# Performance work log

Measured on AMD Instinct MI355X. Metric: run time of the kernel, lower is better.

The kernel has to match this reference:

```python
import jax, jax.numpy as jnp
import numpy as np

NEG_INF = -9e15  # matches the torch -9000000000000000.0 mask value
LRELU_SLOPE = 0.01  # torch nn.LeakyReLU default


def setup_inputs() -> dict:
    key = jax.random.key(0)
    k1, k2, k3, k4 = jax.random.split(key, 4)
    N, F_in, F_out = 8192, 256, 128
    x = jax.random.normal(k1, (N, F_in), dtype=jnp.float32)
    adj = jax.random.randint(k2, (N, N), 0, 2, dtype=jnp.int32)
    # xavier_uniform with gain=1.414
    limW = 1.414 * np.sqrt(6.0 / (F_in + F_out))
    W = jax.random.uniform(k3, (F_in, F_out), minval=-limW, maxval=limW, dtype=jnp.float32)
    lima = 1.414 * np.sqrt(6.0 / (2 * F_out + 1))
    a = jax.random.uniform(k4, (2 * F_out, 1), minval=-lima, maxval=lima, dtype=jnp.float32)
    return {"x": x, "adj": adj, "W": W, "a": a}


def reference(x, adj, W, a):
    # h: [N, F_out]
    h = x @ W
    F_out = h.shape[1]
    a1 = a[:F_out, 0]   # attention vector for source node i
    a2 = a[F_out:, 0]   # attention vector for target node j
    # e[i, j] = leaky_relu(h_i . a1 + h_j . a2) -- equivalent to the repeat/cat
    # construction without materializing the [N, N, 2F] tensor.
    e = (h @ a1)[:, None] + (h @ a2)[None, :]  # [N, N]
    e = jnp.where(e > 0, e, LRELU_SLOPE * e)
    scores = jnp.where(adj > 0, e, NEG_INF)
    attention = jax.nn.softmax(scores, axis=1)  # dropout omitted (eval mode)
    h_prime = attention @ h  # [N, F_out]
    return jax.nn.elu(h_prime)
```

## Files before the change

### kernel.cpp

```cpp
#include <hip/hip_runtime.h>
#include <hip/hip_bf16.h>
#include <stdint.h>


#define N_NODES 8192
#define F_INF   256
#define F_OUT   128
#define LRELU   0.01f

typedef __bf16 bf16x8 __attribute__((ext_vector_type(8)));
typedef float  f32x4  __attribute__((ext_vector_type(4)));
using bf16 = __hip_bfloat16;

__device__ __forceinline__ float b2f(bf16 v) { return __bfloat162float(v); }
__device__ __forceinline__ bf16  f2b(float v) { return __float2bfloat16(v); }

__device__ __forceinline__ void gll16(const void* g, void* l) {
    __builtin_amdgcn_global_load_lds(
        (const __attribute__((address_space(1))) uint32_t*)g,
        (__attribute__((address_space(3))) uint32_t*)l, 16, 0, 0);
}

__global__ __launch_bounds__(256) void k_xw(const float* __restrict__ x,
                                            const float* __restrict__ W,
                                            const float* __restrict__ a,
                                            const int* __restrict__ adjp,
                                            bf16* __restrict__ hT,
                                            float* __restrict__ s1,
                                            float* __restrict__ s2,
                                            float* __restrict__ mgp,
                                            uint32_t* __restrict__ mask) {
    __shared__ __align__(16) bf16 WTh[F_OUT][F_INF + 8];
    __shared__ __align__(16) bf16 WTl[F_OUT][F_INF + 8];
    __shared__ __align__(16) bf16 XSh[32][72];
    __shared__ __align__(16) bf16 XSl[32][72];
    __shared__ float a1s[F_OUT], a2s[F_OUT], s1L[32], s2L[32];
    const int tid  = threadIdx.x;
    const int lane = tid & 63, wave = tid >> 6;
    const int i0   = blockIdx.x * 32;
    if (tid < F_OUT) { a1s[tid] = a[tid]; a2s[tid] = a[tid + F_OUT]; }
    if (tid < 32)    { s1L[tid] = 0.f; s2L[tid] = 0.f; }
    for (int idx = tid; idx < (F_INF * F_OUT) / 8; idx += 256) {
        int k  = idx >> 4;
        int n0 = (idx & 15) * 8;
        const float* src = W + (size_t)k * F_OUT + n0;
        float4 va = *(const float4*)(src);
        float4 vb = *(const float4*)(src + 4);
        float v[8] = {va.x, va.y, va.z, va.w, vb.x, vb.y, vb.z, vb.w};
#pragma unroll
        for (int c = 0; c < 8; ++c) {
            bf16 hi = f2b(v[c]);
            WTh[n0 + c][k] = hi;
            WTl[n0 + c][k] = f2b(v[c] - b2f(hi));
        }
    }
    __syncthreads();
    f32x4 acc[4];
#pragma unroll
    for (int t = 0; t < 4; ++t) acc[t] = {0.f, 0.f, 0.f, 0.f};
    const int m = lane & 15, quad = lane >> 4;
    const int rt = wave & 1, cH = wave >> 1;
    for (int kc = 0; kc < F_INF / 64; ++kc) {
        const int k0 = kc * 64;
        {
            int part = tid & 7;
            int r    = tid >> 3;
            const float* src = x + (size_t)(i0 + r) * F_INF + k0 + part * 8;
            float4 va = *(const float4*)(src);
            float4 vb = *(const float4*)(src + 4);
            float v[8] = {va.x, va.y, va.z, va.w, vb.x, vb.y, vb.z, vb.w};
            __align__(16) bf16 th[8];
            __align__(16) bf16 tl[8];
#pragma unroll
            for (int c = 0; c < 8; ++c) {
                bf16 hi = f2b(v[c]);
                th[c] = hi;
                tl[c] = f2b(v[c] - b2f(hi));
            }
            *(uint4*)(&XSh[r][part * 8]) = *(const uint4*)th;
            *(uint4*)(&XSl[r][part * 8]) = *(const uint4*)tl;
        }
        __syncthreads();
#pragma unroll
        for (int ks = 0; ks < 2; ++ks) {
            bf16x8 ah = *(const bf16x8*)(&XSh[rt * 16 + m][ks * 32 + quad * 8]);
            bf16x8 al = *(const bf16x8*)(&XSl[rt * 16 + m][ks * 32 + quad * 8]);
#pragma unroll
            for (int c = 0; c < 4; ++c) {
                const int ct = cH * 4 + c;
                bf16x8 bh = *(const bf16x8*)(&WTh[ct * 16 + m][k0 + ks * 32 + quad * 8]);
                bf16x8 bl = *(const bf16x8*)(&WTl[ct * 16 + m][k0 + ks * 32 + quad * 8]);
                acc[c] = __builtin_amdgcn_mfma_f32_16x16x32_bf16(al, bh, acc[c], 0, 0, 0);
                acc[c] = __builtin_amdgcn_mfma_f32_16x16x32_bf16(ah, bl, acc[c], 0, 0, 0);
                acc[c] = __builtin_amdgcn_mfma_f32_16x16x32_bf16(ah, bh, acc[c], 0, 0, 0);
            }
        }
        __syncthreads();
    }
    float p1[4] = {0.f, 0.f, 0.f, 0.f}, p2[4] = {0.f, 0.f, 0.f, 0.f};
#pragma unroll
    for (int c = 0; c < 4; ++c) {
        const int f = (cH * 4 + c) * 16 + m;
        const float w1 = a1s[f], w2 = a2s[f];
#pragma unroll
        for (int r = 0; r < 4; ++r) { p1[r] += acc[c][r] * w1; p2[r] += acc[c][r] * w2; }
    }
#pragma unroll
    for (int r = 0; r < 4; ++r) {
        const int row = rt * 16 + quad * 4 + r;
        atomicAdd(&s1L[row], p1[r]);
        atomicAdd(&s2L[row], p2[r]);
    }
#pragma unroll
    for (int c = 0; c < 4; ++c) {
        const int f = (cH * 4 + c) * 16 + m;
#pragma unroll
        for (int r = 0; r < 4; ++r) {
            const int i = i0 + rt * 16 + quad * 4 + r;
            hT[(size_t)f * N_NODES + i] = f2b(acc[c][r]);
        }
    }
    __syncthreads();
    if (tid < 32) {
        s1[i0 + tid] = s1L[tid];
        s2[i0 + tid] = s2L[tid];
        float m2 = s2L[tid];
#pragma unroll
        for (int s = 16; s > 0; s >>= 1) m2 = fmaxf(m2, __shfl_xor(m2, s));
        if (tid == 0) mgp[blockIdx.x] = m2;
    }
    {
        const size_t base = (size_t)blockIdx.x * 8192 + tid;
#pragma unroll 2
        for (int k2 = 0; k2 < 32; ++k2) {
            const size_t w = base + (size_t)k2 * 256;
            const int4* p = (const int4*)(adjp + w * 32);
            uint32_t b = 0;
#pragma unroll
            for (int g = 0; g < 8; ++g) {
                int4 v = p[g];
                b |= (uint32_t)(v.x > 0) << (g * 4 + 0);
                b |= (uint32_t)(v.y > 0) << (g * 4 + 1);
                b |= (uint32_t)(v.z > 0) << (g * 4 + 2);
                b |= (uint32_t)(v.w > 0) << (g * 4 + 3);
            }
            mask[w] = b;
        }
    }
}

__global__ __launch_bounds__(256, 4) void k_attn(const uint32_t* __restrict__ mask,
                                                 const float* __restrict__ s1g,
                                                 const float* __restrict__ s2g,
                                                 const float* __restrict__ mgp,
                                                 const bf16* __restrict__ hT,
                                                 float* __restrict__ Of,
                                                 float* __restrict__ lp) {
    __shared__ __align__(16) bf16 HS2[2][F_OUT][64];
    __shared__ float wred[4];
    __shared__ float lsum[32];
    const int tid  = threadIdx.x;
    const int lane = tid & 63, wave = tid >> 6;
    const int m = lane & 15, quad = lane >> 4;
    const int rt = wave & 1, kh = wave >> 1;
    const int i0    = blockIdx.x * 32;
    const int jq    = blockIdx.y;
    const int jbase = jq * 2048;
    const int irow  = i0 + rt * 16 + m;
    const float s1v = s1g[irow];
    float mv = mgp[tid];
#pragma unroll
    for (int s = 32; s > 0; s >>= 1) mv = fmaxf(mv, __shfl_xor(mv, s));
    if (lane == 0) wred[wave] = mv;
    if (tid < 32) lsum[tid] = 0.f;
    const int part = tid & 7, fr = tid >> 3;
    const int psw  = (part ^ (fr & 7)) * 8;
    const bf16* hTp = hT + jbase + psw;
#pragma unroll
    for (int g = 0; g < 4; ++g)
        gll16(hTp + (size_t)(fr + g * 32) * N_NODES, &HS2[0][fr + g * 32][part * 8]);
    const int jloc = kh * 32 + quad * 8;
    const uint32_t* mrow = mask + (size_t)irow * (N_NODES / 32) + jq * 64;
    const float4*  srowp = (const float4*)(s2g + jbase);
    uint32_t mw = mrow[kh];
    float4 svA = srowp[jloc / 4], svB = srowp[jloc / 4 + 1];
    float lacc = 0.f;
    f32x4 acc[8];
#pragma unroll
    for (int c = 0; c < 8; ++c) acc[c] = {0.f, 0.f, 0.f, 0.f};
    __syncthreads();
    const float mgv = fmaxf(fmaxf(wred[0], wred[1]), fmaxf(wred[2], wred[3]));
    const float tmi = s1v + mgv;
    const float mi  = fmaxf(tmi, LRELU * tmi);
    const int slotsw = ((kh * 4 + quad) ^ (m & 7)) * 8;

    for (int jc = 0; jc < 32; ++jc) {
        const int cur = jc & 1;
        if (jc < 31) {
#pragma unroll
            for (int g = 0; g < 4; ++g)
                gll16(hTp + (size_t)(fr + g * 32) * N_NODES + (jc + 1) * 64,
                      &HS2[cur ^ 1][fr + g * 32][part * 8]);
        }
        const int jn = (jc < 31) ? jc + 1 : 31;
        uint32_t nmw = mrow[jn * 2 + kh];
        float4 nsvA = srowp[jn * 16 + jloc / 4], nsvB = srowp[jn * 16 + jloc / 4 + 1];
        const float sm[8] = {svA.x, svA.y, svA.z, svA.w, svB.x, svB.y, svB.z, svB.w};
        const uint32_t mb = (mw >> (quad * 8)) & 0xffu;
        __align__(16) bf16 a8[8];
#pragma unroll
        for (int t = 0; t < 8; ++t) {
            float e = s1v + sm[t];
            e = fmaxf(e, LRELU * e);
            float w = ((mb >> t) & 1u) ? __expf(e - mi) : 0.f;
            bf16 b = f2b(w);
            a8[t] = b;
            lacc += b2f(b);
        }
        bf16x8 afrag = *(const bf16x8*)a8;
        __builtin_amdgcn_s_setprio(1);
#pragma unroll
        for (int c = 0; c < 8; ++c) {
            bf16x8 bfr = *(const bf16x8*)(&HS2[cur][c * 16 + m][slotsw]);
            acc[c] = __builtin_amdgcn_mfma_f32_16x16x32_bf16(afrag, bfr, acc[c], 0, 0, 0);
        }
        __builtin_amdgcn_s_setprio(0);
        mw = nmw; svA = nsvA; svB = nsvB;
        __syncthreads();
    }
    lacc += __shfl_xor(lacc, 16);
    lacc += __shfl_xor(lacc, 32);
    if (quad == 0) atomicAdd(&lsum[rt * 16 + m], lacc);
    __syncthreads();
    if (tid < 32) lp[(size_t)jq * N_NODES + i0 + tid] = lsum[tid];
    float* scr = (float*)&HS2[0][0][0];
    if (kh == 1) {
#pragma unroll
        for (int c = 0; c < 8; ++c)
#pragma unroll
            for (int r = 0; r < 4; ++r)
                scr[(rt * 16 + quad * 4 + r) * 128 + c * 16 + m] = acc[c][r];
    }
    __syncthreads();
    if (kh == 0) {
#pragma unroll
        for (int c = 0; c < 8; ++c)
#pragma unroll
            for (int r = 0; r < 4; ++r) {
                const int row = rt * 16 + quad * 4 + r;
                const int f   = c * 16 + m;
                Of[((size_t)jq * N_NODES + i0 + row) * F_OUT + f] =
                    acc[c][r] + scr[row * 128 + f];
            }
    }
}

__global__ __launch_bounds__(256) void k_comb(const float* __restrict__ Of,
                                              const float* __restrict__ lp,
                                              float* __restrict__ out) {
    size_t gid = (size_t)blockIdx.x * 256 + threadIdx.x;
    int i = (int)(gid >> 7);
    float s = 0.f, l = 0.f;
#pragma unroll
    for (int q = 0; q < 4; ++q) {
        s += Of[(size_t)q * (N_NODES * (size_t)F_OUT) + gid];
        l += lp[q * N_NODES + i];
    }
    float o = s / l;
    out[gid] = o > 0.f ? o : __expf(o) - 1.f;
}

extern "C" void kernel_launch(void* const* d_in, const int* in_sizes, int n_in,
                              void* d_out, int out_size, void* d_ws, size_t ws_size,
                              hipStream_t stream) {
    (void)out_size; (void)ws_size;
    const float* x   = nullptr;
    const int*   adj = nullptr;
    const float* W   = nullptr;
    const float* a   = nullptr;
    for (int ii = 0; ii < n_in; ++ii) {
        int sz = in_sizes[ii];
        if      (sz == N_NODES * F_INF)  x   = (const float*)d_in[ii];
        else if (sz == F_INF * F_OUT)    W   = (const float*)d_in[ii];
        else if (sz == 2 * F_OUT)        a   = (const float*)d_in[ii];
        else                             adj = (const int*)d_in[ii];
    }
    float* out = (float*)d_out;

    char* ws = (char*)d_ws;
    bf16*     hT   = (bf16*)ws;     ws += (size_t)F_OUT * N_NODES * 2;
    float*    s1   = (float*)ws;    ws += N_NODES * 4;
    float*    s2   = (float*)ws;    ws += N_NODES * 4;
    float*    mgp  = (float*)ws;    ws += 256 * 4;
    float*    lp   = (float*)ws;    ws += 4 * N_NODES * 4;
    uint32_t* mask = (uint32_t*)ws;
    ws += (size_t)N_NODES * (N_NODES / 32) * sizeof(uint32_t);
    float*    Of   = (float*)ws;

    k_xw  <<<N_NODES / 32, 256, 0, stream>>>(x, W, a, adj, hT, s1, s2, mgp, mask);
    k_attn<<<dim3(N_NODES / 32, 4), 256, 0, stream>>>(mask, s1, s2, mgp, hT, Of, lp);
    k_comb<<<(N_NODES * F_OUT) / 256, 256, 0, stream>>>(Of, lp, out);
}
```

Before: 441.6 us.

## Remove j-split in attention kernel and fuse final combine with ELU

The attention kernel now processes the full neighbor range per row block instead of splitting it four ways. Normalization and ELU are applied directly in the epilogue, which eliminates the partial output buffers and the separate combine kernel launch. This removes the partial-result write and read traffic and one launch. The grid shrinks fourfold to roughly one block per CU, which reduces parallelism and latency hiding.

```diff
diff --git a/kernel.cpp b/kernel.cpp
--- a/kernel.cpp
+++ b/kernel.cpp
@@ -154,8 +154,7 @@
                                                  const float* __restrict__ s2g,
                                                  const float* __restrict__ mgp,
                                                  const bf16* __restrict__ hT,
-                                                 float* __restrict__ Of,
-                                                 float* __restrict__ lp) {
+                                                 float* __restrict__ out) {
     __shared__ __align__(16) bf16 HS2[2][F_OUT][64];
     __shared__ float wred[4];
     __shared__ float lsum[32];
@@ -163,10 +162,8 @@
     const int lane = tid & 63, wave = tid >> 6;
     const int m = lane & 15, quad = lane >> 4;
     const int rt = wave & 1, kh = wave >> 1;
-    const int i0    = blockIdx.x * 32;
-    const int jq    = blockIdx.y;
-    const int jbase = jq * 2048;
-    const int irow  = i0 + rt * 16 + m;
+    const int i0   = blockIdx.x * 32;
+    const int irow = i0 + rt * 16 + m;
     const float s1v = s1g[irow];
     float mv = mgp[tid];
 #pragma unroll
@@ -175,13 +172,13 @@
     if (tid < 32) lsum[tid] = 0.f;
     const int part = tid & 7, fr = tid >> 3;
     const int psw  = (part ^ (fr & 7)) * 8;
-    const bf16* hTp = hT + jbase + psw;
+    const bf16* hTp = hT + psw;
 #pragma unroll
     for (int g = 0; g < 4; ++g)
         gll16(hTp + (size_t)(fr + g * 32) * N_NODES, &HS2[0][fr + g * 32][part * 8]);
     const int jloc = kh * 32 + quad * 8;
-    const uint32_t* mrow = mask + (size_t)irow * (N_NODES / 32) + jq * 64;
-    const float4*  srowp = (const float4*)(s2g + jbase);
+    const uint32_t* mrow = mask + (size_t)irow * (N_NODES / 32);
+    const float4*  srowp = (const float4*)(s2g);
     uint32_t mw = mrow[kh];
     float4 svA = srowp[jloc / 4], svB = srowp[jloc / 4 + 1];
     float lacc = 0.f;
@@ -194,15 +191,15 @@
     const float mi  = fmaxf(tmi, LRELU * tmi);
     const int slotsw = ((kh * 4 + quad) ^ (m & 7)) * 8;
 
-    for (int jc = 0; jc < 32; ++jc) {
+    for (int jc = 0; jc < 128; ++jc) {
         const int cur = jc & 1;
-        if (jc < 31) {
+        if (jc < 127) {
 #pragma unroll
             for (int g = 0; g < 4; ++g)
                 gll16(hTp + (size_t)(fr + g * 32) * N_NODES + (jc + 1) * 64,
                       &HS2[cur ^ 1][fr + g * 32][part * 8]);
         }
-        const int jn = (jc < 31) ? jc + 1 : 31;
+        const int jn = (jc < 127) ? jc + 1 : 127;
         uint32_t nmw = mrow[jn * 2 + kh];
         float4 nsvA = srowp[jn * 16 + jloc / 4], nsvB = srowp[jn * 16 + jloc / 4 + 1];
         const float sm[8] = {svA.x, svA.y, svA.z, svA.w, svB.x, svB.y, svB.z, svB.w};
@@ -232,7 +229,6 @@
     lacc += __shfl_xor(lacc, 32);
     if (quad == 0) atomicAdd(&lsum[rt * 16 + m], lacc);
     __syncthreads();
-    if (tid < 32) lp[(size_t)jq * N_NODES + i0 + tid] = lsum[tid];
     float* scr = (float*)&HS2[0][0][0];
     if (kh == 1) {
 #pragma unroll
@@ -249,25 +245,10 @@
             for (int r = 0; r < 4; ++r) {
                 const int row = rt * 16 + quad * 4 + r;
                 const int f   = c * 16 + m;
-                Of[((size_t)jq * N_NODES + i0 + row) * F_OUT + f] =
-                    acc[c][r] + scr[row * 128 + f];
-            }
-    }
-}
-
-__global__ __launch_bounds__(256) void k_comb(const float* __restrict__ Of,
-                                              const float* __restrict__ lp,
-                                              float* __restrict__ out) {
-    size_t gid = (size_t)blockIdx.x * 256 + threadIdx.x;
-    int i = (int)(gid >> 7);
-    float s = 0.f, l = 0.f;
-#pragma unroll
-    for (int q = 0; q < 4; ++q) {
-        s += Of[(size_t)q * (N_NODES * (size_t)F_OUT) + gid];
-        l += lp[q * N_NODES + i];
-    }
-    float o = s / l;
-    out[gid] = o > 0.f ? o : __expf(o) - 1.f;
+                const float o = (acc[c][r] + scr[row * 128 + f]) / lsum[row];
+                out[(size_t)(i0 + row) * F_OUT + f] = o > 0.f ? o : __expf(o) - 1.f;
+            }
+    }
 }
 
 extern "C" void kernel_launch(void* const* d_in, const int* in_sizes, int n_in,
@@ -292,12 +273,9 @@
     float*    s1   = (float*)ws;    ws += N_NODES * 4;
     float*    s2   = (float*)ws;    ws += N_NODES * 4;
     float*    mgp  = (float*)ws;    ws += 256 * 4;
-    float*    lp   = (float*)ws;    ws += 4 * N_NODES * 4;
     uint32_t* mask = (uint32_t*)ws;
     ws += (size_t)N_NODES * (N_NODES / 32) * sizeof(uint32_t);
-    float*    Of   = (float*)ws;
 
     k_xw  <<<N_NODES / 32, 256, 0, stream>>>(x, W, a, adj, hT, s1, s2, mgp, mask);
-    k_attn<<<dim3(N_NODES / 32, 4), 256, 0, stream>>>(mask, s1, s2, mgp, hT, Of, lp);
-    k_comb<<<(N_NODES * F_OUT) / 256, 256, 0, stream>>>(Of, lp, out);
-}
+    k_attn<<<N_NODES / 32, 256, 0, stream>>>(mask, s1, s2, mgp, hT, out);
+}
```

Result: slower. 507.3 us (+14.9%).

## Load hT fragments directly from global into registers instead of LDS staging

Applied to the files above, without the earlier changes.

Removes the double-buffered LDS staging of hT tiles with global_load_lds and the per-iteration __syncthreads. Each wave now loads its B fragments for the MFMA directly from global memory into registers every chunk. This drops barrier and LDS-traffic cost. In exchange, each rtile pair loads the same hT data redundantly, the 16-byte loads are strided by N_NODES rows, and load latency is exposed inside the loop without explicit prefetching.

```diff
diff --git a/kernel.cpp b/kernel.cpp
--- a/kernel.cpp
+++ b/kernel.cpp
@@ -14,12 +14,6 @@
 
 __device__ __forceinline__ float b2f(bf16 v) { return __bfloat162float(v); }
 __device__ __forceinline__ bf16  f2b(float v) { return __float2bfloat16(v); }
-
-__device__ __forceinline__ void gll16(const void* g, void* l) {
-    __builtin_amdgcn_global_load_lds(
-        (const __attribute__((address_space(1))) uint32_t*)g,
-        (__attribute__((address_space(3))) uint32_t*)l, 16, 0, 0);
-}
 
 __global__ __launch_bounds__(256) void k_xw(const float* __restrict__ x,
                                             const float* __restrict__ W,
@@ -156,7 +150,7 @@
                                                  const bf16* __restrict__ hT,
                                                  float* __restrict__ Of,
                                                  float* __restrict__ lp) {
-    __shared__ __align__(16) bf16 HS2[2][F_OUT][64];
+    __shared__ float scr[32 * 128];
     __shared__ float wred[4];
     __shared__ float lsum[32];
     const int tid  = threadIdx.x;
@@ -173,12 +167,6 @@
     for (int s = 32; s > 0; s >>= 1) mv = fmaxf(mv, __shfl_xor(mv, s));
     if (lane == 0) wred[wave] = mv;
     if (tid < 32) lsum[tid] = 0.f;
-    const int part = tid & 7, fr = tid >> 3;
-    const int psw  = (part ^ (fr & 7)) * 8;
-    const bf16* hTp = hT + jbase + psw;
-#pragma unroll
-    for (int g = 0; g < 4; ++g)
-        gll16(hTp + (size_t)(fr + g * 32) * N_NODES, &HS2[0][fr + g * 32][part * 8]);
     const int jloc = kh * 32 + quad * 8;
     const uint32_t* mrow = mask + (size_t)irow * (N_NODES / 32) + jq * 64;
     const float4*  srowp = (const float4*)(s2g + jbase);
@@ -192,19 +180,16 @@
     const float mgv = fmaxf(fmaxf(wred[0], wred[1]), fmaxf(wred[2], wred[3]));
     const float tmi = s1v + mgv;
     const float mi  = fmaxf(tmi, LRELU * tmi);
-    const int slotsw = ((kh * 4 + quad) ^ (m & 7)) * 8;
+    const bf16* hTl = hT + jbase + jloc;
 
     for (int jc = 0; jc < 32; ++jc) {
-        const int cur = jc & 1;
-        if (jc < 31) {
-#pragma unroll
-            for (int g = 0; g < 4; ++g)
-                gll16(hTp + (size_t)(fr + g * 32) * N_NODES + (jc + 1) * 64,
-                      &HS2[cur ^ 1][fr + g * 32][part * 8]);
-        }
         const int jn = (jc < 31) ? jc + 1 : 31;
         uint32_t nmw = mrow[jn * 2 + kh];
         float4 nsvA = srowp[jn * 16 + jloc / 4], nsvB = srowp[jn * 16 + jloc / 4 + 1];
+        bf16x8 bfr[8];
+#pragma unroll
+        for (int c = 0; c < 8; ++c)
+            bfr[c] = *(const bf16x8*)(hTl + (size_t)(c * 16 + m) * N_NODES + jc * 64);
         const float sm[8] = {svA.x, svA.y, svA.z, svA.w, svB.x, svB.y, svB.z, svB.w};
         const uint32_t mb = (mw >> (quad * 8)) & 0xffu;
         __align__(16) bf16 a8[8];
@@ -220,20 +205,16 @@
         bf16x8 afrag = *(const bf16x8*)a8;
         __builtin_amdgcn_s_setprio(1);
 #pragma unroll
-        for (int c = 0; c < 8; ++c) {
-            bf16x8 bfr = *(const bf16x8*)(&HS2[cur][c * 16 + m][slotsw]);
-            acc[c] = __builtin_amdgcn_mfma_f32_16x16x32_bf16(afrag, bfr, acc[c], 0, 0, 0);
-        }
+        for (int c = 0; c < 8; ++c)
+            acc[c] = __builtin_amdgcn_mfma_f32_16x16x32_bf16(afrag, bfr[c], acc[c], 0, 0, 0);
         __builtin_amdgcn_s_setprio(0);
         mw = nmw; svA = nsvA; svB = nsvB;
-        __syncthreads();
     }
     lacc += __shfl_xor(lacc, 16);
     lacc += __shfl_xor(lacc, 32);
     if (quad == 0) atomicAdd(&lsum[rt * 16 + m], lacc);
     __syncthreads();
     if (tid < 32) lp[(size_t)jq * N_NODES + i0 + tid] = lsum[tid];
-    float* scr = (float*)&HS2[0][0][0];
     if (kh == 1) {
 #pragma unroll
         for (int c = 0; c < 8; ++c)
```

After: 527.7 us. 19.5% more time.
